# Kernel tuning notes

Measured on AMD Instinct MI355X. Metric: run time of the kernel, lower is better.

Reference implementation:

```python
import jax, jax.numpy as jnp
import numpy as np

NUM_HEADS = 12
EMBED_DIM = 768
HEAD_DIM = EMBED_DIM // NUM_HEADS


def setup_inputs() -> dict:
    key = jax.random.key(0)
    ks = jax.random.split(key, 9)
    B, S, D = 8, 1025, EMBED_DIM
    s = 1.0 / np.sqrt(D)
    return {
        "x": jax.random.normal(ks[0], (B, S, D), dtype=jnp.float32),
        "Wk": jax.random.normal(ks[1], (D, D), dtype=jnp.float32) * s,
        "bk": jnp.zeros((D,), dtype=jnp.float32),
        "Wq": jax.random.normal(ks[2], (D, D), dtype=jnp.float32) * s,
        "bq": jnp.zeros((D,), dtype=jnp.float32),
        "Wv": jax.random.normal(ks[3], (D, D), dtype=jnp.float32) * s,
        "bv": jnp.zeros((D,), dtype=jnp.float32),
        "Wp": jax.random.normal(ks[4], (D, D), dtype=jnp.float32) * s,
        "bp": jnp.zeros((D,), dtype=jnp.float32),
    }


def reference(x, Wk, bk, Wq, bq, Wv, bv, Wp, bp):
    B, S, D = x.shape
    H, Hd = NUM_HEADS, HEAD_DIM
    # Linear projections (torch Linear: y = x @ W^T + b)
    k = (x @ Wk.T + bk).reshape(B, S, H, Hd).transpose(0, 2, 1, 3)  # (B,H,S,Hd)
    q = (x @ Wq.T + bq).reshape(B, S, H, Hd).transpose(0, 2, 1, 3)
    v = (x @ Wv.T + bv).reshape(B, S, H, Hd).transpose(0, 2, 1, 3)
    scale = 1.0 / jnp.sqrt(jnp.asarray(Hd, dtype=x.dtype))
    scores = jnp.einsum("bhqd,bhkd->bhqk", q, k) * scale  # (B,H,S,S)
    attn = jax.nn.softmax(scores, axis=-1)
    # dropout is identity at inference (eval mode)
    out = jnp.einsum("bhqk,bhkd->bhqd", attn, v)  # (B,H,S,Hd)
    out = out.transpose(0, 2, 1, 3).reshape(B, S, D)
    return out @ Wp.T + bp
```

## Files before the change

### kernel.cpp

```cpp
#include <hip/hip_runtime.h>
#include <stdint.h>

#define BATCH  8
#define SEQ    1025
#define DMODEL 768
#define NHEAD  12
#define HDIM   64
#define MTOT   (BATCH * SEQ)
#define MPAD   8320
#define SPAD   1056
#define BHTOT  (BATCH * NHEAD)
#define QT32   33
#define NTILE  17
#define NKSTEP 12
#define QKSCALE 0.18033688011112042f

typedef __bf16 bf16x8 __attribute__((ext_vector_type(8)));
typedef __bf16 bf16x4 __attribute__((ext_vector_type(4)));
typedef float  f32x4  __attribute__((ext_vector_type(4)));
typedef float  f32x16 __attribute__((ext_vector_type(16)));

#if __has_builtin(__builtin_amdgcn_exp2f)
#define EXP2F __builtin_amdgcn_exp2f
#else
#define EXP2F exp2f
#endif

constexpr size_t XB_OFF  = 0;
constexpr size_t XB_SZ   = (size_t)MPAD * DMODEL * 2;
constexpr size_t W_SZ    = (size_t)DMODEL * DMODEL * 2;
constexpr size_t WQB_OFF = XB_OFF + XB_SZ;
constexpr size_t WKB_OFF = WQB_OFF + W_SZ;
constexpr size_t WVB_OFF = WKB_OFF + W_SZ;
constexpr size_t WPB_OFF = WVB_OFF + W_SZ;
constexpr size_t QB_OFF  = WPB_OFF + W_SZ;
constexpr size_t QB_SZ   = (size_t)BHTOT * SEQ * HDIM * 2;
constexpr size_t KB_OFF  = QB_OFF + QB_SZ;
constexpr size_t VT_OFF  = KB_OFF + QB_SZ;
constexpr size_t VT_SZ   = (size_t)BHTOT * HDIM * SPAD * 2;
constexpr size_t AO_OFF  = XB_OFF;
constexpr size_t WS_NEEDED = VT_OFF + VT_SZ;

__device__ __forceinline__ void async16(const void* g, void* l) {
  __builtin_amdgcn_global_load_lds((__attribute__((address_space(1))) void*)g,
                                   (__attribute__((address_space(3))) void*)l,
                                   16, 0, 0);
}

__device__ __forceinline__ unsigned pkbf(float lo, float hi) {
  __bf16 l = (__bf16)lo, h = (__bf16)hi;
  unsigned short lb = __builtin_bit_cast(unsigned short, l);
  unsigned short hb = __builtin_bit_cast(unsigned short, h);
  return ((unsigned)hb << 16) | (unsigned)lb;
}
__device__ __forceinline__ unsigned shfl32u(unsigned x) {
  return (unsigned)__shfl_xor((int)x, 32, 64);
}
__device__ __forceinline__ float pairmax(float x) {
  return fmaxf(x, __shfl_xor(x, 32, 64));
}
__device__ __forceinline__ float pairsum(float x) {
  return x + __shfl_xor(x, 32, 64);
}

__device__ __forceinline__ float tree_max16(const f32x16& s) {
  float a0 = fmaxf(s[0], s[1]),   a1 = fmaxf(s[2], s[3]);
  float a2 = fmaxf(s[4], s[5]),   a3 = fmaxf(s[6], s[7]);
  float a4 = fmaxf(s[8], s[9]),   a5 = fmaxf(s[10], s[11]);
  float a6 = fmaxf(s[12], s[13]), a7 = fmaxf(s[14], s[15]);
  float b0 = fmaxf(a0, a1), b1 = fmaxf(a2, a3);
  float b2 = fmaxf(a4, a5), b3 = fmaxf(a6, a7);
  return fmaxf(fmaxf(b0, b1), fmaxf(b2, b3));
}
__device__ __forceinline__ float tree_sum16(const f32x16& s) {
  float a0 = s[0] + s[1],   a1 = s[2] + s[3];
  float a2 = s[4] + s[5],   a3 = s[6] + s[7];
  float a4 = s[8] + s[9],   a5 = s[10] + s[11];
  float a6 = s[12] + s[13], a7 = s[14] + s[15];
  float b0 = a0 + a1, b1 = a2 + a3, b2 = a4 + a5, b3 = a6 + a7;
  return (b0 + b1) + (b2 + b3);
}

__global__ void __launch_bounds__(256)
convert_f32_bf16(const float* __restrict__ src, __bf16* __restrict__ dst,
                 int n_src, int n_dst) {
  int idx = (blockIdx.x * 256 + threadIdx.x) * 4;
  if (idx >= n_dst) return;
  bf16x4 o;
  if (idx + 3 < n_src) {
    float4 v = *(const float4*)&src[idx];
    o[0] = (__bf16)v.x; o[1] = (__bf16)v.y; o[2] = (__bf16)v.z; o[3] = (__bf16)v.w;
  } else {
    #pragma unroll
    for (int t = 0; t < 4; ++t) {
      int k = idx + t;
      o[t] = (k < n_src) ? (__bf16)src[k] : (__bf16)0.f;
    }
  }
  *(bf16x4*)&dst[idx] = o;
}

__global__ void __launch_bounds__(256)
convert_w4(const float* __restrict__ w0, const float* __restrict__ w1,
           const float* __restrict__ w2, const float* __restrict__ w3,
           __bf16* __restrict__ dst) {
  const int which = blockIdx.y;
  const float* src = (which == 0) ? w0 : (which == 1) ? w1 : (which == 2) ? w2 : w3;
  __bf16* d = dst + (size_t)which * DMODEL * DMODEL;
  int idx = (blockIdx.x * 256 + threadIdx.x) * 4;
  if (idx >= DMODEL * DMODEL) return;
  float4 v = *(const float4*)&src[idx];
  bf16x4 o;
  o[0] = (__bf16)v.x; o[1] = (__bf16)v.y; o[2] = (__bf16)v.z; o[3] = (__bf16)v.w;
  *(bf16x4*)&d[idx] = o;
}

__device__ __forceinline__ void stage_step(const __bf16* const (&sa)[4],
                                           const __bf16* const (&sw)[4],
                                           __bf16* As, __bf16* Bs,
                                           int kt, int tid) {
  #pragma unroll
  for (int i = 0; i < 4; ++i) {
    const int gi = i * 256 + tid;
    async16(sa[i] + kt, As + gi * 8);
    async16(sw[i] + kt, Bs + gi * 8);
  }
}

__device__ __forceinline__ void compute_tile(const __bf16* __restrict__ pa,
                                             const __bf16* __restrict__ pb,
                                             int off0, int off1,
                                             f32x4 acc[4][4]) {
  #pragma unroll
  for (int kk = 0; kk < 2; ++kk) {
    const int offk = kk ? off1 : off0;
    bf16x8 af[4], bfr[4];
    #pragma unroll
    for (int i = 0; i < 4; ++i)
      af[i] = *(const bf16x8*)(pa + i * 1024 + offk);
    #pragma unroll
    for (int j = 0; j < 4; ++j)
      bfr[j] = *(const bf16x8*)(pb + j * 1024 + offk);
    __builtin_amdgcn_s_setprio(1);
    #pragma unroll
    for (int i = 0; i < 4; ++i)
      #pragma unroll
      for (int j = 0; j < 4; ++j)
        acc[i][j] = __builtin_amdgcn_mfma_f32_16x16x32_bf16(af[i], bfr[j], acc[i][j], 0, 0, 0);
    __builtin_amdgcn_s_setprio(0);
  }
}

#define GC_WAIT8  asm volatile("s_waitcnt vmcnt(8)" ::: "memory")
#define GC_WAIT0  asm volatile("s_waitcnt vmcnt(0)" ::: "memory")
#define GC_BAR    __builtin_amdgcn_s_barrier()
#define GC_SCHED  __builtin_amdgcn_sched_barrier(0)

__device__ __forceinline__ void gemm_core(const __bf16* __restrict__ A,
                                          const __bf16* __restrict__ W,
                                          __bf16 (*As)[128 * 64], __bf16 (*Bs)[128 * 64],
                                          int m0, int n0, f32x4 acc[4][4]) {
  const int tid  = threadIdx.x;
  const int lane = tid & 63;
  const int wave = tid >> 6;
  const int wm = wave >> 1, wn = wave & 1;
  const int l15 = lane & 15, lg = lane >> 4;
  const int rx  = l15 & 7;

  const __bf16* sa[4];
  const __bf16* sw[4];
  #pragma unroll
  for (int i = 0; i < 4; ++i) {
    const int gi = i * 256 + tid;
    const int r  = gi >> 3;
    const int g  = (gi & 7) ^ (r & 7);
    sa[i] = A + (size_t)(m0 + r) * DMODEL + g * 8;
    sw[i] = W + (size_t)(n0 + r) * DMODEL + g * 8;
  }
  const int off0 = ((0 * 4 + lg) ^ rx) * 8;
  const int off1 = ((1 * 4 + lg) ^ rx) * 8;
  const __bf16* paA0 = &As[0][(wm * 64 + l15) * 64];
  const __bf16* paA1 = &As[1][(wm * 64 + l15) * 64];
  const __bf16* pbB0 = &Bs[0][(wn * 64 + l15) * 64];
  const __bf16* pbB1 = &Bs[1][(wn * 64 + l15) * 64];

  stage_step(sa, sw, As[0], Bs[0], 0, tid);

  #pragma unroll 1
  for (int tt = 0; tt < NKSTEP / 2; ++tt) {
    const int t = tt * 2;
    stage_step(sa, sw, As[1], Bs[1], (t + 1) * 64, tid);
    GC_WAIT8;
    GC_BAR;
    GC_SCHED;
    compute_tile(paA0, pbB0, off0, off1, acc);
    GC_BAR;
    GC_SCHED;
    if (t + 2 < NKSTEP) {
      stage_step(sa, sw, As[0], Bs[0], (t + 2) * 64, tid);
      GC_WAIT8;
    } else {
      GC_WAIT0;
    }
    GC_BAR;
    GC_SCHED;
    compute_tile(paA1, pbB1, off0, off1, acc);
    GC_BAR;
    GC_SCHED;
  }
}

__global__ void __launch_bounds__(256)
gemm_qkv_kernel(const __bf16* __restrict__ xb, const __bf16* __restrict__ wsb,
                const float* __restrict__ bq, const float* __restrict__ bk,
                const float* __restrict__ bv,
                __bf16* __restrict__ qb, __bf16* __restrict__ kb,
                __bf16* __restrict__ vtb) {
  __shared__ __bf16 As[2][128 * 64];
  __shared__ __bf16 Bs[2][128 * 64];
  const int wg  = blockIdx.x;
  const int xcd = wg & 7, idx = wg >> 3;
  const int v   = xcd * 146 + (xcd < 2 ? xcd : 2) + idx;
  const int m0  = (v / 18) * 128;
  const int n0  = (v % 18) * 128;

  f32x4 acc[4][4];
  #pragma unroll
  for (int i = 0; i < 4; ++i)
    #pragma unroll
    for (int j = 0; j < 4; ++j) acc[i][j] = (f32x4){0.f, 0.f, 0.f, 0.f};

  gemm_core(xb, wsb, As, Bs, m0, n0, acc);

  const int lane = threadIdx.x & 63;
  const int wave = threadIdx.x >> 6;
  const int wm = wave >> 1, wn = wave & 1;
  const int l15 = lane & 15, lg = lane >> 4;
  #pragma unroll
  for (int i = 0; i < 4; ++i) {
    #pragma unroll
    for (int j = 0; j < 4; ++j) {
      const int ncolg = n0 + wn * 64 + j * 16 + l15;
      const int mode = ncolg / 768;
      const int col  = ncolg - mode * 768;
      const float bb = (mode == 0 ? bq : (mode == 1 ? bk : bv))[col];
      const int h = col >> 6, hd = col & 63;
      #pragma unroll
      for (int r = 0; r < 4; ++r) {
        const int mrow = m0 + wm * 64 + i * 16 + lg * 4 + r;
        if (mrow < MTOT) {
          float val = acc[i][j][r] + bb;
          const int b = mrow / SEQ;
          const int s = mrow - b * SEQ;
          const int bh = b * NHEAD + h;
          if (mode == 2)
            vtb[((size_t)bh * HDIM + hd) * SPAD + s] = (__bf16)val;
          else if (mode == 0)
            qb[((size_t)bh * SEQ + s) * HDIM + hd] = (__bf16)(val * QKSCALE);
          else
            kb[((size_t)bh * SEQ + s) * HDIM + hd] = (__bf16)val;
        }
      }
    }
  }
}

__global__ void __launch_bounds__(256)
gemm_proj_kernel(const __bf16* __restrict__ ab, const __bf16* __restrict__ wpb,
                 const float* __restrict__ bp, float* __restrict__ out) {
  __shared__ __bf16 As[2][128 * 64];
  __shared__ __bf16 Bs[2][128 * 64];
  const int wg  = blockIdx.x;
  const int xcd = wg & 7, idx = wg >> 3;
  const int v   = xcd * 48 + (xcd < 6 ? xcd : 6) + idx;
  const int m0  = (v / 6) * 128;
  const int n0  = (v % 6) * 128;

  f32x4 acc[4][4];
  #pragma unroll
  for (int i = 0; i < 4; ++i)
    #pragma unroll
    for (int j = 0; j < 4; ++j) acc[i][j] = (f32x4){0.f, 0.f, 0.f, 0.f};

  gemm_core(ab, wpb, As, Bs, m0, n0, acc);

  const int lane = threadIdx.x & 63;
  const int wave = threadIdx.x >> 6;
  const int wm = wave >> 1, wn = wave & 1;
  const int l15 = lane & 15, lg = lane >> 4;
  #pragma unroll
  for (int i = 0; i < 4; ++i) {
    #pragma unroll
    for (int j = 0; j < 4; ++j) {
      const int ncol = n0 + wn * 64 + j * 16 + l15;
      const float bb = bp[ncol];
      #pragma unroll
      for (int r = 0; r < 4; ++r) {
        const int mrow = m0 + wm * 64 + i * 16 + lg * 4 + r;
        if (mrow < MTOT) out[(size_t)mrow * DMODEL + ncol] = acc[i][j][r] + bb;
      }
    }
  }
}

__device__ __forceinline__ void build_pa(const f32x16& s, int hi, bf16x8 pa[2]) {
  #pragma unroll
  for (int sl2 = 0; sl2 < 2; ++sl2) {
    const int off = sl2 * 8;
    unsigned w0 = pkbf(s[off + 0], s[off + 1]);
    unsigned w1 = pkbf(s[off + 2], s[off + 3]);
    unsigned w2 = pkbf(s[off + 4], s[off + 5]);
    unsigned w3 = pkbf(s[off + 6], s[off + 7]);
    unsigned p0 = shfl32u(w0), p1 = shfl32u(w1);
    unsigned p2 = shfl32u(w2), p3 = shfl32u(w3);
    unsigned pw[4];
    pw[0] = hi ? p2 : w0;
    pw[1] = hi ? p3 : w1;
    pw[2] = hi ? w2 : p0;
    pw[3] = hi ? w3 : p1;
    __builtin_memcpy(&pa[sl2], pw, 16);
  }
}

__device__ __forceinline__ void stage_kv(const __bf16* __restrict__ Kp,
                                         const __bf16* __restrict__ Vp,
                                         __bf16* kls, __bf16* vls,
                                         int k0, int tid) {
  const int r = tid >> 3, p = tid & 7;
  const int g = p ^ (r & 7);
  async16(Kp + (size_t)(k0 + r) * HDIM + g * 8, kls + tid * 8);
  int col = k0 + g * 8;
  if (col >= SPAD) col = 0;
  async16(Vp + (size_t)r * SPAD + col, vls + tid * 8);
}

template<bool MASK>
__device__ __forceinline__ void attn_step(const __bf16* __restrict__ kls,
                                          const __bf16* __restrict__ vls,
                                          int half, const bf16x8 (&qf)[4],
                                          int l31, int hi,
                                          float& mrun, float& lrun,
                                          f32x16& o0, f32x16& o1) {
  const int kr = half * 32 + l31;
  const int krx = kr & 7;

  f32x16 s;
  #pragma unroll
  for (int r = 0; r < 16; ++r) s[r] = 0.f;
  #pragma unroll
  for (int sl = 0; sl < 4; ++sl) {
    bf16x8 kf = *(const bf16x8*)&kls[(kr * 8 + ((2 * sl + hi) ^ krx)) * 8];
    s = __builtin_amdgcn_mfma_f32_32x32x16_bf16(kf, qf[sl], s, 0, 0, 0);
  }
  if (MASK) {
    #pragma unroll
    for (int r = 1; r < 16; ++r) s[r] = -1e30f;
    if (hi) s[0] = -1e30f;
  }

  const float mloc = pairmax(tree_max16(s));
  if (!__all(mloc - mrun <= 8.f)) {
    const float mnew = fmaxf(mrun, mloc);
    const float corr = EXP2F(mrun - mnew);
    lrun *= corr;
    #pragma unroll
    for (int r = 0; r < 16; ++r) { o0[r] *= corr; o1[r] *= corr; }
    mrun = mnew;
  }

  #pragma unroll
  for (int r = 0; r < 16; ++r) s[r] = EXP2F(s[r] - mrun);
  lrun += pairsum(tree_sum16(s));

  bf16x8 pa[2];
  build_pa(s, hi, pa);

  #pragma unroll
  for (int ot = 0; ot < 2; ++ot) {
    const int vr = ot * 32 + l31;
    const int vrx = vr & 7;
    f32x16& o = ot ? o1 : o0;
    #pragma unroll
    for (int j = 0; j < 2; ++j) {
      bf16x8 vf = *(const bf16x8*)&vls[(vr * 8 + ((half * 4 + 2 * j + hi) ^ vrx)) * 8];
      o = __builtin_amdgcn_mfma_f32_32x32x16_bf16(vf, pa[j], o, 0, 0, 0);
    }
  }
}

__global__ void __launch_bounds__(512, 4)
attn_kernel(const __bf16* __restrict__ qb, const __bf16* __restrict__ kb,
            const __bf16* __restrict__ vtb, __bf16* __restrict__ ao) {
  __shared__ __bf16 kls[2][64 * 64];
  __shared__ __bf16 vls[2][64 * 64];

  const int tid  = threadIdx.x;
  const int wid  = tid >> 6;
  const int lane = tid & 63;
  const int l31 = lane & 31, hi = (lane >> 5) & 1;

  const int bid = blockIdx.x;
  const int xcd = bid & 7;
  const int ixd = bid >> 3;
  const int bh  = xcd * (BHTOT / 8) + ixd / 5;
  const int qblk = ixd % 5;
  const int qt  = qblk * 8 + wid;
  const bool active = qt < QT32;

  const __bf16* Qp = qb + (size_t)bh * SEQ * HDIM;
  const __bf16* Kp = kb + (size_t)bh * SEQ * HDIM;
  const __bf16* Vp = vtb + (size_t)bh * HDIM * SPAD;

  const int qidx = qt * 32 + l31;
  const int qc = (qidx < SEQ ? qidx : SEQ - 1);
  bf16x8 qf[4];
  if (active) {
    #pragma unroll
    for (int sl = 0; sl < 4; ++sl)
      qf[sl] = *(const bf16x8*)&Qp[(size_t)qc * HDIM + sl * 16 + hi * 8];
  }

  f32x16 o0, o1;
  #pragma unroll
  for (int r = 0; r < 16; ++r) { o0[r] = 0.f; o1[r] = 0.f; }
  float mrun = -1e30f, lrun = 0.f;

  stage_kv(Kp, Vp, kls[0], vls[0], 0, tid);
  __syncthreads();

  for (int t = 0; t < NTILE; ++t) {
    const int cur = t & 1;
    if (t + 1 < NTILE)
      stage_kv(Kp, Vp, kls[cur ^ 1], vls[cur ^ 1], (t + 1) * 64, tid);
    if (active) {
      if (t < NTILE - 1) {
        attn_step<false>(kls[cur], vls[cur], 0, qf, l31, hi, mrun, lrun, o0, o1);
        attn_step<false>(kls[cur], vls[cur], 1, qf, l31, hi, mrun, lrun, o0, o1);
      } else {
        attn_step<true>(kls[cur], vls[cur], 0, qf, l31, hi, mrun, lrun, o0, o1);
      }
    }
    __syncthreads();
  }

  if (active && qidx < SEQ) {
    const int b = bh / NHEAD, h = bh % NHEAD;
    const float inv = 1.f / lrun;
    __bf16* base = ao + ((size_t)b * SEQ + qidx) * DMODEL + h * HDIM + hi * 4;
    #pragma unroll
    for (int t = 0; t < 2; ++t) {
      const f32x16& o = t ? o1 : o0;
      #pragma unroll
      for (int g = 0; g < 4; ++g) {
        bf16x4 w;
        #pragma unroll
        for (int u = 0; u < 4; ++u) w[u] = (__bf16)(o[g * 4 + u] * inv);
        *(bf16x4*)(base + t * 32 + g * 8) = w;
      }
    }
  }
}

extern "C" void kernel_launch(void* const* d_in, const int* in_sizes, int n_in,
                              void* d_out, int out_size, void* d_ws, size_t ws_size,
                              hipStream_t stream) {
  const float* x  = (const float*)d_in[0];
  const float* Wk = (const float*)d_in[1];
  const float* bk = (const float*)d_in[2];
  const float* Wq = (const float*)d_in[3];
  const float* bq = (const float*)d_in[4];
  const float* Wv = (const float*)d_in[5];
  const float* bv = (const float*)d_in[6];
  const float* Wp = (const float*)d_in[7];
  const float* bp = (const float*)d_in[8];
  float* out = (float*)d_out;

  if (ws_size < WS_NEEDED) return;

  char* ws = (char*)d_ws;
  __bf16* xb  = (__bf16*)(ws + XB_OFF);
  __bf16* wqb = (__bf16*)(ws + WQB_OFF);
  __bf16* wpb = (__bf16*)(ws + WPB_OFF);
  __bf16* qb  = (__bf16*)(ws + QB_OFF);
  __bf16* kb  = (__bf16*)(ws + KB_OFF);
  __bf16* vtb = (__bf16*)(ws + VT_OFF);
  __bf16* ab  = (__bf16*)(ws + AO_OFF);

  hipMemsetAsync(vtb, 0, VT_SZ, stream);

  {
    const int n_src = MTOT * DMODEL, n_dst = MPAD * DMODEL;
    convert_f32_bf16<<<dim3((n_dst / 4 + 255) / 256), dim3(256), 0, stream>>>(x, xb, n_src, n_dst);
    const int nw = DMODEL * DMODEL;
    convert_w4<<<dim3((nw / 4 + 255) / 256, 4), dim3(256), 0, stream>>>(Wq, Wk, Wv, Wp, wqb);
  }

  gemm_qkv_kernel<<<dim3(1170), dim3(256), 0, stream>>>(
      xb, wqb, bq, bk, bv, qb, kb, vtb);

  attn_kernel<<<dim3(8 * (BHTOT / 8) * 5), dim3(512), 0, stream>>>(qb, kb, vtb, ab);

  gemm_proj_kernel<<<dim3(390), dim3(256), 0, stream>>>(ab, wpb, bp, out);
}
```

Measured before the change: 171.8 us.

## Interleave async global-to-LDS staging with MFMA sub-phases in GEMM main loop

Restructures the double-buffered GEMM K-loop so each k-tile's compute is split into four MFMA sub-phases. Each sub-phase issues a slice of the next B tile, or of the A tile two steps ahead, as async loads, with barriers between phases. The prologue prefetches A for two tiles and B for one. The aim is to spread memory traffic across the compute and shorten the vmcnt waits before barriers. The cost is more barriers per tile and a more intricate buffer-reuse schedule that must be correct.

```diff
diff --git a/kernel.cpp b/kernel.cpp
--- a/kernel.cpp
+++ b/kernel.cpp
@@ -115,46 +115,97 @@
   *(bf16x4*)&d[idx] = o;
 }
 
-__device__ __forceinline__ void stage_step(const __bf16* const (&sa)[4],
-                                           const __bf16* const (&sw)[4],
-                                           __bf16* As, __bf16* Bs,
-                                           int kt, int tid) {
-  #pragma unroll
-  for (int i = 0; i < 4; ++i) {
-    const int gi = i * 256 + tid;
-    async16(sa[i] + kt, As + gi * 8);
-    async16(sw[i] + kt, Bs + gi * 8);
-  }
-}
-
-__device__ __forceinline__ void compute_tile(const __bf16* __restrict__ pa,
-                                             const __bf16* __restrict__ pb,
-                                             int off0, int off1,
-                                             f32x4 acc[4][4]) {
-  #pragma unroll
-  for (int kk = 0; kk < 2; ++kk) {
-    const int offk = kk ? off1 : off0;
-    bf16x8 af[4], bfr[4];
-    #pragma unroll
-    for (int i = 0; i < 4; ++i)
-      af[i] = *(const bf16x8*)(pa + i * 1024 + offk);
-    #pragma unroll
-    for (int j = 0; j < 4; ++j)
-      bfr[j] = *(const bf16x8*)(pb + j * 1024 + offk);
-    __builtin_amdgcn_s_setprio(1);
-    #pragma unroll
-    for (int i = 0; i < 4; ++i)
-      #pragma unroll
-      for (int j = 0; j < 4; ++j)
-        acc[i][j] = __builtin_amdgcn_mfma_f32_16x16x32_bf16(af[i], bfr[j], acc[i][j], 0, 0, 0);
-    __builtin_amdgcn_s_setprio(0);
-  }
-}
-
-#define GC_WAIT8  asm volatile("s_waitcnt vmcnt(8)" ::: "memory")
+#define GC_WAIT4  asm volatile("s_waitcnt vmcnt(4)" ::: "memory")
 #define GC_WAIT0  asm volatile("s_waitcnt vmcnt(0)" ::: "memory")
 #define GC_BAR    __builtin_amdgcn_s_barrier()
 #define GC_SCHED  __builtin_amdgcn_sched_barrier(0)
+#define MFMA16(a, b, c) __builtin_amdgcn_mfma_f32_16x16x32_bf16((a), (b), (c), 0, 0, 0)
+
+__device__ __forceinline__ void tile4(const __bf16* __restrict__ pa,
+                                      const __bf16* __restrict__ pb,
+                                      __bf16* bnext,
+                                      __bf16* aself,
+                                      const __bf16* const (&sa)[4],
+                                      const __bf16* const (&sw)[4],
+                                      int t, int off0, int off1, int tid,
+                                      f32x4 acc[4][4]) {
+  const bool stgB = (t + 1) < NKSTEP;
+  const bool stgA = (t + 2) < NKSTEP;
+  bf16x8 af0[4], af1[4];
+
+  if (stgB) {
+    async16(sw[0] + (t + 1) * 64, bnext + (0 * 256 + tid) * 8);
+    async16(sw[1] + (t + 1) * 64, bnext + (1 * 256 + tid) * 8);
+  }
+  {
+    bf16x8 b0 = *(const bf16x8*)(pb + 0 * 1024 + off0);
+    bf16x8 b1 = *(const bf16x8*)(pb + 1 * 1024 + off0);
+    #pragma unroll
+    for (int i = 0; i < 4; ++i) af0[i] = *(const bf16x8*)(pa + i * 1024 + off0);
+    __builtin_amdgcn_s_setprio(1);
+    #pragma unroll
+    for (int i = 0; i < 4; ++i) {
+      acc[i][0] = MFMA16(af0[i], b0, acc[i][0]);
+      acc[i][1] = MFMA16(af0[i], b1, acc[i][1]);
+    }
+    __builtin_amdgcn_s_setprio(0);
+  }
+  GC_BAR; GC_SCHED;
+
+  if (stgB) {
+    async16(sw[2] + (t + 1) * 64, bnext + (2 * 256 + tid) * 8);
+    async16(sw[3] + (t + 1) * 64, bnext + (3 * 256 + tid) * 8);
+  }
+  {
+    bf16x8 b0 = *(const bf16x8*)(pb + 0 * 1024 + off1);
+    bf16x8 b1 = *(const bf16x8*)(pb + 1 * 1024 + off1);
+    #pragma unroll
+    for (int i = 0; i < 4; ++i) af1[i] = *(const bf16x8*)(pa + i * 1024 + off1);
+    __builtin_amdgcn_s_setprio(1);
+    #pragma unroll
+    for (int i = 0; i < 4; ++i) {
+      acc[i][0] = MFMA16(af1[i], b0, acc[i][0]);
+      acc[i][1] = MFMA16(af1[i], b1, acc[i][1]);
+    }
+    __builtin_amdgcn_s_setprio(0);
+  }
+  GC_BAR; GC_SCHED;
+
+  if (stgA) {
+    async16(sa[0] + (t + 2) * 64, aself + (0 * 256 + tid) * 8);
+    async16(sa[1] + (t + 2) * 64, aself + (1 * 256 + tid) * 8);
+  }
+  {
+    bf16x8 b2 = *(const bf16x8*)(pb + 2 * 1024 + off0);
+    bf16x8 b3 = *(const bf16x8*)(pb + 3 * 1024 + off0);
+    __builtin_amdgcn_s_setprio(1);
+    #pragma unroll
+    for (int i = 0; i < 4; ++i) {
+      acc[i][2] = MFMA16(af0[i], b2, acc[i][2]);
+      acc[i][3] = MFMA16(af0[i], b3, acc[i][3]);
+    }
+    __builtin_amdgcn_s_setprio(0);
+  }
+  GC_BAR; GC_SCHED;
+
+  if (stgA) {
+    async16(sa[2] + (t + 2) * 64, aself + (2 * 256 + tid) * 8);
+    async16(sa[3] + (t + 2) * 64, aself + (3 * 256 + tid) * 8);
+  }
+  {
+    bf16x8 b2 = *(const bf16x8*)(pb + 2 * 1024 + off1);
+    bf16x8 b3 = *(const bf16x8*)(pb + 3 * 1024 + off1);
+    __builtin_amdgcn_s_setprio(1);
+    #pragma unroll
+    for (int i = 0; i < 4; ++i) {
+      acc[i][2] = MFMA16(af1[i], b2, acc[i][2]);
+      acc[i][3] = MFMA16(af1[i], b3, acc[i][3]);
+    }
+    __builtin_amdgcn_s_setprio(0);
+  }
+  if (stgA) { GC_WAIT4; } else { GC_WAIT0; }
+  GC_BAR; GC_SCHED;
+}
 
 __device__ __forceinline__ void gemm_core(const __bf16* __restrict__ A,
                                           const __bf16* __restrict__ W,
@@ -179,34 +230,24 @@
   }
   const int off0 = ((0 * 4 + lg) ^ rx) * 8;
   const int off1 = ((1 * 4 + lg) ^ rx) * 8;
-  const __bf16* paA0 = &As[0][(wm * 64 + l15) * 64];
-  const __bf16* paA1 = &As[1][(wm * 64 + l15) * 64];
-  const __bf16* pbB0 = &Bs[0][(wn * 64 + l15) * 64];
-  const __bf16* pbB1 = &Bs[1][(wn * 64 + l15) * 64];
-
-  stage_step(sa, sw, As[0], Bs[0], 0, tid);
+  const int paoff = (wm * 64 + l15) * 64;
+  const int pboff = (wn * 64 + l15) * 64;
+
+  #pragma unroll
+  for (int i = 0; i < 4; ++i) {
+    async16(sa[i], As[0] + (i * 256 + tid) * 8);
+    async16(sw[i], Bs[0] + (i * 256 + tid) * 8);
+  }
+  #pragma unroll
+  for (int i = 0; i < 4; ++i)
+    async16(sa[i] + 64, As[1] + (i * 256 + tid) * 8);
+  GC_WAIT4; GC_BAR; GC_SCHED;
 
   #pragma unroll 1
   for (int tt = 0; tt < NKSTEP / 2; ++tt) {
     const int t = tt * 2;
-    stage_step(sa, sw, As[1], Bs[1], (t + 1) * 64, tid);
-    GC_WAIT8;
-    GC_BAR;
-    GC_SCHED;
-    compute_tile(paA0, pbB0, off0, off1, acc);
-    GC_BAR;
-    GC_SCHED;
-    if (t + 2 < NKSTEP) {
-      stage_step(sa, sw, As[0], Bs[0], (t + 2) * 64, tid);
-      GC_WAIT8;
-    } else {
-      GC_WAIT0;
-    }
-    GC_BAR;
-    GC_SCHED;
-    compute_tile(paA1, pbB1, off0, off1, acc);
-    GC_BAR;
-    GC_SCHED;
+    tile4(&As[0][paoff], &Bs[0][pboff], Bs[1], As[0], sa, sw, t,     off0, off1, tid, acc);
+    tile4(&As[1][paoff], &Bs[1][pboff], Bs[0], As[1], sa, sw, t + 1, off0, off1, tid, acc);
   }
 }
 
```

Result: slower. 182.4 us (+6.2%).
